# Kernel tuning notes

Hardware: AMD Instinct MI355X
Metric: run time of the kernel (lower is better)

The kernel has to match this reference:

```python
import jax, jax.numpy as jnp
import numpy as np

B, NJ, NM = 64, 30, 20
N = NJ * NM          # 600 operation nodes per FJSP instance
IN_DIM, H = 2, 128


def _bn(h):
    # torch BatchNorm1d in training mode, gamma=1/beta=0 (module init), stats over all nodes
    m = h.mean(axis=(0, 1))
    v = h.var(axis=(0, 1))
    return (h - m) / jnp.sqrt(v + 1e-5)


def setup_inputs() -> dict:
    key = jax.random.key(0)
    ks = jax.random.split(key, 20)
    x = jax.random.normal(ks[0], (B, N, IN_DIM), jnp.float32)
    graph_pool = jnp.full((B, N), 1.0 / N, jnp.float32)   # average graph pooling weights
    padded_nei = jnp.zeros((1,), jnp.int32)               # unused (sum pooling path)
    adj = (jax.random.uniform(ks[1], (B, N, N)) < 0.01).astype(jnp.float32)
    adj = jnp.minimum(adj + jnp.eye(N, dtype=jnp.float32)[None], 1.0)  # self-loops
    candidate = jax.random.randint(ks[2], (B, NJ), 0, N)
    a_index = jax.random.randint(ks[3], (B,), 0, NJ)
    mask = jax.random.uniform(ks[4], (B, NJ)) < 0.2
    mask = mask.at[jnp.arange(B), a_index].set(False)     # chosen action never masked
    mask_mch = jax.random.uniform(ks[5], (B, N, NM)) < 0.3
    dur = jax.random.uniform(ks[6], (B, N, NM), dtype=jnp.float32)
    old_action = jax.random.randint(ks[7], (B,), 0, N)
    mch_pool = jax.random.normal(ks[8], (B, H), jnp.float32)

    def w(k, i, o):
        return jax.random.normal(k, (i, o), jnp.float32) * (1.0 / np.sqrt(i))

    z = lambda n: jnp.zeros((n,), jnp.float32)            # biases init to 0 in module
    return dict(
        x=x, graph_pool=graph_pool, padded_nei=padded_nei, adj=adj,
        candidate=candidate, mask=mask, mask_mch=mask_mch, dur=dur,
        a_index=a_index, old_action=old_action, mch_pool=mch_pool,
        W1_0=w(ks[9], IN_DIM, H), b1_0=z(H), W2_0=w(ks[10], H, H), b2_0=z(H),
        W1_1=w(ks[11], H, H), b1_1=z(H), W2_1=w(ks[12], H, H), b2_1=z(H),
        Wa1=w(ks[13], 3 * H, H), ba1=z(H), Wa2=w(ks[14], H, H), ba2=z(H),
        Wa3=w(ks[15], H, 1), ba3=z(1),
        Wc1=w(ks[16], H, H), bc1=z(H), Wc2=w(ks[17], H, 1), bc2=z(1),
    )


def reference(x, graph_pool, padded_nei, adj, candidate, mask, mask_mch, dur,
              a_index, old_action, mch_pool,
              W1_0, b1_0, W2_0, b2_0, W1_1, b1_1, W2_1, b2_1,
              Wa1, ba1, Wa2, ba2, Wa3, ba3, Wc1, bc1, Wc2, bc2):
    # --- GIN encoder: num_layers-1 = 2 message-passing layers, sum pooling ---
    h = x
    for (W1, b1, W2, b2) in ((W1_0, b1_0, W2_0, b2_0), (W1_1, b1_1, W2_1, b2_1)):
        pooled = jnp.einsum('bnm,bmd->bnd', adj, h)         # neighbor sum (adj has self-loops)
        h1 = jax.nn.relu(_bn(pooled @ W1 + b1))             # MLP hidden (BN inside MLP)
        h = jax.nn.relu(_bn(h1 @ W2 + b2))                  # layer BN + relu
    h_nodes = h                                             # [B, N, H]
    h_pooled = jnp.einsum('bn,bnd->bd', graph_pool, h_nodes)  # [B, H]

    # --- gather candidate features, concat pooled contexts ---
    cand_feat = jnp.take_along_axis(h_nodes, candidate[:, :, None], axis=1)  # [B, NJ, H]
    concat = jnp.concatenate([
        cand_feat,
        jnp.broadcast_to(h_pooled[:, None, :], cand_feat.shape),
        jnp.broadcast_to(mch_pool[:, None, :], cand_feat.shape)], axis=-1)   # [B, NJ, 3H]

    # --- MLPActor(3 layers, tanh) ---
    a = jnp.tanh(concat @ Wa1 + ba1)
    a = jnp.tanh(a @ Wa2 + ba2)
    scores = (a @ Wa3 + ba3).squeeze(-1) * 10.0             # [B, NJ]
    scores = jnp.where(mask, -jnp.inf, scores)
    logpi = jax.nn.log_softmax(scores, axis=1)
    pi = jnp.exp(logpi)
    log_a = jnp.take_along_axis(logpi, a_index[:, None], axis=1)[:, 0]
    entropy = -jnp.sum(jnp.where(pi > 0, pi * logpi, 0.0), axis=1)

    # --- gather action-dependent tensors (detached in torch) ---
    b_idx = jnp.arange(B)
    action_node = dur[b_idx, old_action]                    # [B, NM]
    action_feature = h_nodes[b_idx, old_action]             # [B, H]
    mask_mch_action = mask_mch[b_idx, old_action][:, None, :]  # [B, 1, NM]

    # --- MLPCritic(2 layers, tanh) ---
    v = jnp.tanh(h_pooled @ Wc1 + bc1) @ Wc2 + bc2          # [B, 1]

    sg = jax.lax.stop_gradient
    return (entropy, v, log_a, sg(action_node), sg(action_feature),
            mask_mch_action, sg(h_pooled))
```

## Files before the change

### kernel.cpp

```cpp
#include <hip/hip_runtime.h>
#include <hip/hip_bf16.h>

#define BB 64
#define NJ 30
#define NM 20
#define NN 600
#define HH 128
#define NROWS (BB*NN)
#define CAP 48

typedef __attribute__((ext_vector_type(8))) short short8;
typedef __attribute__((ext_vector_type(4))) float f32x4;

#define STATS_B   0
#define HPOOL_B   4096
#define FLAGS_B   36864
#define ZERO_B    36880
#define WTB_B     37120
#define SCORES_B  135424
#define NBRCNT_B  143104
#define NBRIDX_B  296704
#define CONCAT_B  296704
#define A1_B      3245824
#define POOLED0_B 7669504
#define T1_B      7976704
#define P1_B      27637504

#define OUT_ENT   0
#define OUT_V     64
#define OUT_LOGA  128
#define OUT_ANODE 192
#define OUT_AFEAT 1472
#define OUT_MMCH  9664
#define OUT_HPOOL 10944

__device__ __forceinline__ bool mask_at(const void* p, int layout, long i) {
    if (layout == 2) return ((const float*)p)[i] != 0.f;
    if (layout == 1) return ((const unsigned char*)p)[i] != 0;
    return ((const int*)p)[i] != 0;
}

__device__ __forceinline__ short bf16rne(float f) {
    unsigned u = __float_as_uint(f);
    return (short)((u + 0x7fffu + ((u >> 16) & 1u)) >> 16);
}
__device__ __forceinline__ float bf2f(unsigned h) {
    return __uint_as_float(h << 16);
}
__device__ __forceinline__ unsigned packbf(float a, float b) {
    return ((unsigned)(unsigned short)bf16rne(a)) |
           (((unsigned)(unsigned short)bf16rne(b)) << 16);
}

__global__ __launch_bounds__(256) void k_detect(const void* mask_p, const void* maskmch_p,
                                                int* flags) {
    unsigned agg = 0;
    int which;
    int tid = threadIdx.x;
    if (blockIdx.x == 0) {
        which = 0;
        const unsigned* p = (const unsigned*)mask_p;
        unsigned w0 = (tid < 480) ? p[tid] : 0u;
        unsigned w1 = (tid + 256 < 480) ? p[tid + 256] : 0u;
        agg = w0 | w1;
    } else {
        which = 1;
        const unsigned* p = (const unsigned*)maskmch_p + (size_t)(blockIdx.x - 1) * 800;
        unsigned w0 = p[tid];
        unsigned w1 = (tid + 256 < 800) ? p[tid + 256] : 0u;
        unsigned w2 = (tid + 512 < 800) ? p[tid + 512] : 0u;
        unsigned w3 = (tid + 768 < 800) ? p[tid + 768] : 0u;
        agg = w0 | w1 | w2 | w3;
    }
    int f = 0;
    if (((agg >> 24) & 0xffu) == 0x3fu) f |= 1;
    if ((((agg >> 8) & 0xffu) == 1u) || (((agg >> 16) & 0xffu) == 1u) ||
        (((agg >> 24) & 0xffu) == 1u)) f |= 2;
#pragma unroll
    for (int off = 1; off < 64; off <<= 1) f |= __shfl_xor(f, off);
    if ((tid & 63) == 0 && f) atomicOr(&flags[which], f);
}

__global__ void k_wconv(const float* __restrict__ Wa, const float* __restrict__ Wb,
                        const float* __restrict__ Wc, unsigned short* __restrict__ wT) {
    int mat = blockIdx.x >> 6;
    int idx = ((blockIdx.x & 63) << 8) + threadIdx.x;
    const float* W = mat == 0 ? Wa : (mat == 1 ? Wb : Wc);
    int k = idx >> 7, c = idx & 127;
    wT[mat * 16384 + c * HH + k] = (unsigned short)bf16rne(W[idx]);
}

__global__ __launch_bounds__(256) void k_sparse(const float* __restrict__ adj,
                                                const float* __restrict__ x,
                                                int* __restrict__ nbr_cnt,
                                                int* __restrict__ nbr_idx,
                                                float* __restrict__ pooled0) {
    int wrow = blockIdx.x * 4 + (threadIdx.x >> 6);
    int lane = threadIdx.x & 63;
    int b = wrow / NN;
    const float4* arow = (const float4*)(adj + (size_t)wrow * NN);
    int* irow = nbr_idx + (size_t)wrow * CAP;
    const float* xb = x + (size_t)b * NN * 2;
    float4 vv[3];
    vv[0] = arow[lane];
    vv[1] = arow[64 + lane];
    vv[2] = (128 + lane < 150) ? arow[128 + lane] : make_float4(0.f, 0.f, 0.f, 0.f);
    int cnt = 0;
    float p0 = 0.f, p1 = 0.f;
#pragma unroll
    for (int it = 0; it < 3; ++it) {
        int fi = it * 64 + lane;
#pragma unroll
        for (int s = 0; s < 4; ++s) {
            float c = s == 0 ? vv[it].x : (s == 1 ? vv[it].y : (s == 2 ? vv[it].z : vv[it].w));
            bool pred = (c != 0.f);
            unsigned long long bal = __ballot(pred);
            if (pred) {
                int pos = cnt + __popcll(bal & ((1ull << lane) - 1ull));
                int m = fi * 4 + s;
                if (pos < CAP) irow[pos] = m;
                float2 xv = *(const float2*)&xb[m * 2];
                p0 += xv.x; p1 += xv.y;
            }
            cnt += __popcll(bal);
        }
    }
#pragma unroll
    for (int off = 1; off < 64; off <<= 1) {
        p0 += __shfl_xor(p0, off);
        p1 += __shfl_xor(p1, off);
    }
    if (lane == 0) {
        nbr_cnt[wrow] = cnt < CAP ? cnt : CAP;
        pooled0[(size_t)wrow * 2]     = p0;
        pooled0[(size_t)wrow * 2 + 1] = p1;
    }
}

__global__ __launch_bounds__(256) void k_p0stats(const float* __restrict__ pooled0,
                                                 float* __restrict__ out5) {
    __shared__ float red[4][5];
    int i = blockIdx.x * 256 + threadIdx.x;
    float p0 = pooled0[(size_t)i * 2], p1 = pooled0[(size_t)i * 2 + 1];
    float v[5] = {p0, p1, p0 * p0, p1 * p1, p0 * p1};
#pragma unroll
    for (int j = 0; j < 5; ++j)
#pragma unroll
        for (int off = 1; off < 64; off <<= 1) v[j] += __shfl_xor(v[j], off);
    int lane = threadIdx.x & 63, w = threadIdx.x >> 6;
    if (lane == 0)
#pragma unroll
        for (int j = 0; j < 5; ++j) red[w][j] = v[j];
    __syncthreads();
    if (threadIdx.x == 0)
#pragma unroll
        for (int j = 0; j < 5; ++j)
            atomicAdd(&out5[j], red[0][j] + red[1][j] + red[2][j] + red[3][j]);
}

template<int MODE, int OUTBF>
__global__ __launch_bounds__(256) void k_stage(const void* __restrict__ t_in_v,
                                               const float* __restrict__ pooled0,
                                               const float* __restrict__ W1,
                                               const unsigned short* __restrict__ wT,
                                               const float* __restrict__ stats_in,
                                               void* __restrict__ t_out_v,
                                               float* __restrict__ stats_out) {
    __shared__ float sm_mean[HH], sm_inv[HH];
    __shared__ float smS[4][HH], smQ[4][HH];
    int tid = threadIdx.x;
    if (MODE == 0 && tid < HH) {
        float S0 = stats_in[0], S1 = stats_in[1], Q0 = stats_in[2], Q1 = stats_in[3], P01 = stats_in[4];
        float w0 = W1[tid], w1 = W1[HH + tid];
        float m = (S0 * w0 + S1 * w1) * (1.f / NROWS);
        float eq = (Q0 * w0 * w0 + Q1 * w1 * w1 + 2.f * P01 * w0 * w1) * (1.f / NROWS);
        sm_mean[tid] = m;
        sm_inv[tid] = 1.f / sqrtf(eq - m * m + 1e-5f);
    }
    if (MODE == 1 && tid < HH) {
        float s = stats_in[tid], q = stats_in[HH + tid];
        float m = s * (1.f / NROWS);
        sm_mean[tid] = m;
        sm_inv[tid] = 1.f / sqrtf(q * (1.f / NROWS) - m * m + 1e-5f);
    }
    if (MODE != 2) __syncthreads();

    const unsigned short* tin = (const unsigned short*)t_in_v;
    int lane = tid & 63, wave = tid >> 6;
    int r16 = lane & 15, kg = lane >> 4;
    int rowbase = blockIdx.x * 64 + wave * 16;

    f32x4 acc[8];
#pragma unroll
    for (int t = 0; t < 8; ++t)
#pragma unroll
        for (int i = 0; i < 4; ++i) acc[t][i] = 0.f;

    float p0 = 0.f, p1 = 0.f;
    if (MODE == 0) {
        p0 = pooled0[(size_t)(rowbase + r16) * 2];
        p1 = pooled0[(size_t)(rowbase + r16) * 2 + 1];
    }

#pragma unroll
    for (int ks = 0; ks < 4; ++ks) {
        int kb = ks * 32 + kg * 8;
        short8 afr;
        if (MODE == 2) {
            afr = *(const short8*)&tin[(size_t)(rowbase + r16) * HH + kb];
        } else {
            float av[8];
            if (MODE == 0) {
                float4 wa0 = *(const float4*)&W1[kb];
                float4 wa1 = *(const float4*)&W1[kb + 4];
                float4 wb0 = *(const float4*)&W1[HH + kb];
                float4 wb1 = *(const float4*)&W1[HH + kb + 4];
                av[0] = p0 * wa0.x + p1 * wb0.x; av[1] = p0 * wa0.y + p1 * wb0.y;
                av[2] = p0 * wa0.z + p1 * wb0.z; av[3] = p0 * wa0.w + p1 * wb0.w;
                av[4] = p0 * wa1.x + p1 * wb1.x; av[5] = p0 * wa1.y + p1 * wb1.y;
                av[6] = p0 * wa1.z + p1 * wb1.z; av[7] = p0 * wa1.w + p1 * wb1.w;
            } else {
                short8 raw = *(const short8*)&tin[(size_t)(rowbase + r16) * HH + kb];
#pragma unroll
                for (int j = 0; j < 8; ++j) av[j] = bf2f((unsigned short)raw[j]);
            }
            float4 m0 = *(const float4*)&sm_mean[kb];
            float4 m1 = *(const float4*)&sm_mean[kb + 4];
            float4 i0 = *(const float4*)&sm_inv[kb];
            float4 i1 = *(const float4*)&sm_inv[kb + 4];
            av[0] = fmaxf((av[0] - m0.x) * i0.x, 0.f);
            av[1] = fmaxf((av[1] - m0.y) * i0.y, 0.f);
            av[2] = fmaxf((av[2] - m0.z) * i0.z, 0.f);
            av[3] = fmaxf((av[3] - m0.w) * i0.w, 0.f);
            av[4] = fmaxf((av[4] - m1.x) * i1.x, 0.f);
            av[5] = fmaxf((av[5] - m1.y) * i1.y, 0.f);
            av[6] = fmaxf((av[6] - m1.z) * i1.z, 0.f);
            av[7] = fmaxf((av[7] - m1.w) * i1.w, 0.f);
#pragma unroll
            for (int j = 0; j < 8; ++j) afr[j] = bf16rne(av[j]);
        }
#pragma unroll
        for (int t = 0; t < 8; ++t) {
            short8 bfr = *(const short8*)&wT[(size_t)(t * 16 + r16) * HH + kb];
            acc[t] = __builtin_amdgcn_mfma_f32_16x16x32_bf16(afr, bfr, acc[t], 0, 0, 0);
        }
    }

#pragma unroll
    for (int t = 0; t < 8; ++t) {
        int col = t * 16 + r16;
        float s = 0.f, q = 0.f;
#pragma unroll
        for (int i = 0; i < 4; ++i) {
            float v = acc[t][i];
            if (OUTBF)
                ((unsigned short*)t_out_v)[(size_t)(rowbase + kg * 4 + i) * HH + col] =
                    (unsigned short)bf16rne(v);
            else
                ((float*)t_out_v)[(size_t)(rowbase + kg * 4 + i) * HH + col] = v;
            s += v; q += v * v;
        }
        s += __shfl_xor(s, 16); q += __shfl_xor(q, 16);
        s += __shfl_xor(s, 32); q += __shfl_xor(q, 32);
        if (kg == 0) { smS[wave][col] = s; smQ[wave][col] = q; }
    }
    __syncthreads();
    if (tid < HH) {
        atomicAdd(&stats_out[tid],      smS[0][tid] + smS[1][tid] + smS[2][tid] + smS[3][tid]);
        atomicAdd(&stats_out[HH + tid], smQ[0][tid] + smQ[1][tid] + smQ[2][tid] + smQ[3][tid]);
    }
}

__global__ __launch_bounds__(256) void k_pool1(const unsigned short* __restrict__ t1,
                                               const int* __restrict__ nbr_cnt,
                                               const int* __restrict__ nbr_idx,
                                               const float* __restrict__ stats1,
                                               unsigned short* __restrict__ pooled1) {
    __shared__ float sm_mean[HH], sm_inv[HH];
    int tid = threadIdx.x;
    if (tid < HH) {
        float s = stats1[tid], q = stats1[HH + tid];
        float m = s * (1.f / NROWS);
        sm_mean[tid] = m;
        sm_inv[tid] = 1.f / sqrtf(q * (1.f / NROWS) - m * m + 1e-5f);
    }
    __syncthreads();
    int c4 = tid & 31, rl = tid >> 5;
    int row = blockIdx.x * 8 + rl;
    int b = row / NN;
    float4 mm = *(const float4*)&sm_mean[c4 * 4];
    float4 iv = *(const float4*)&sm_inv[c4 * 4];
    int cnt = nbr_cnt[row];
    const int* ir = nbr_idx + (size_t)row * CAP;
    const unsigned short* tb = t1 + (size_t)b * NN * HH;
    float a0 = 0.f, a1 = 0.f, a2 = 0.f, a3 = 0.f;
    int i = 0;
    for (; i + 1 < cnt; i += 2) {
        int m0 = ir[i], m1 = ir[i + 1];
        uint2 w0 = *(const uint2*)&tb[(size_t)m0 * HH + c4 * 4];
        uint2 w1 = *(const uint2*)&tb[(size_t)m1 * HH + c4 * 4];
        a0 += fmaxf((bf2f(w0.x & 0xffffu) - mm.x) * iv.x, 0.f)
            + fmaxf((bf2f(w1.x & 0xffffu) - mm.x) * iv.x, 0.f);
        a1 += fmaxf((bf2f(w0.x >> 16)     - mm.y) * iv.y, 0.f)
            + fmaxf((bf2f(w1.x >> 16)     - mm.y) * iv.y, 0.f);
        a2 += fmaxf((bf2f(w0.y & 0xffffu) - mm.z) * iv.z, 0.f)
            + fmaxf((bf2f(w1.y & 0xffffu) - mm.z) * iv.z, 0.f);
        a3 += fmaxf((bf2f(w0.y >> 16)     - mm.w) * iv.w, 0.f)
            + fmaxf((bf2f(w1.y >> 16)     - mm.w) * iv.w, 0.f);
    }
    if (i < cnt) {
        int m0 = ir[i];
        uint2 w0 = *(const uint2*)&tb[(size_t)m0 * HH + c4 * 4];
        a0 += fmaxf((bf2f(w0.x & 0xffffu) - mm.x) * iv.x, 0.f);
        a1 += fmaxf((bf2f(w0.x >> 16)     - mm.y) * iv.y, 0.f);
        a2 += fmaxf((bf2f(w0.y & 0xffffu) - mm.z) * iv.z, 0.f);
        a3 += fmaxf((bf2f(w0.y >> 16)     - mm.w) * iv.w, 0.f);
    }
    uint2 o;
    o.x = packbf(a0, a1);
    o.y = packbf(a2, a3);
    *(uint2*)&pooled1[(size_t)row * HH + c4 * 4] = o;
}

__global__ __launch_bounds__(256) void k_hpool(const float* __restrict__ t3,
                                               const float* __restrict__ gp,
                                               const float* __restrict__ stats3,
                                               float* __restrict__ hpool) {
    __shared__ float sm_mean[HH], sm_inv[HH];
    __shared__ float red[256];
    int tid = threadIdx.x;
    if (tid < HH) {
        float s = stats3[tid], q = stats3[HH + tid];
        float m = s * (1.f / NROWS);
        sm_mean[tid] = m;
        sm_inv[tid] = 1.f / sqrtf(q * (1.f / NROWS) - m * m + 1e-5f);
    }
    __syncthreads();
    int b = blockIdx.x >> 3, chunk = blockIdx.x & 7;
    int c = tid & 127, rr = tid >> 7;
    float m = sm_mean[c], iv = sm_inv[c];
    float acc = 0.f;
    for (int n = chunk * 75 + rr; n < chunk * 75 + 75; n += 2) {
        float w = gp[b * NN + n];
        float v = t3[((size_t)b * NN + n) * HH + c];
        acc += w * fmaxf((v - m) * iv, 0.f);
    }
    red[tid] = acc;
    __syncthreads();
    if (tid < HH) atomicAdd(&hpool[b * HH + c], red[c] + red[c + 128]);
}

__global__ __launch_bounds__(128) void k_concat(const float* __restrict__ t3,
                                                const int* __restrict__ cand,
                                                const float* __restrict__ hpool,
                                                const float* __restrict__ mch,
                                                const float* __restrict__ stats3,
                                                float* __restrict__ concat) {
    __shared__ float sm_mean[HH], sm_inv[HH];
    int t = threadIdx.x;
    {
        float s = stats3[t], q = stats3[HH + t];
        float m = s * (1.f / NROWS);
        sm_mean[t] = m;
        sm_inv[t] = 1.f / sqrtf(q * (1.f / NROWS) - m * m + 1e-5f);
    }
    __syncthreads();
    int row = blockIdx.x;
    int b = row / NJ;
    int cd = cand[row];
    float v = t3[((size_t)b * NN + cd) * HH + t];
    concat[(size_t)row * 384 + t]       = fmaxf((v - sm_mean[t]) * sm_inv[t], 0.f);
    concat[(size_t)row * 384 + 128 + t] = hpool[b * HH + t];
    concat[(size_t)row * 384 + 256 + t] = mch[b * HH + t];
}

__global__ __launch_bounds__(256) void k_a1(const float* __restrict__ concat,
                                            const float* __restrict__ Wa1,
                                            const float* __restrict__ ba1,
                                            float* __restrict__ a1out) {
    __shared__ float sh[8 * 384];
    int tid = threadIdx.x;
    int rbase = blockIdx.x * 8;
    const float4* src = (const float4*)(concat + (size_t)rbase * 384);
    float4* dst = (float4*)sh;
    for (int i = tid; i < 768; i += 256) dst[i] = src[i];
    __syncthreads();
    int c = tid & 127, slot = tid >> 7;
    float acc[4] = {0.f, 0.f, 0.f, 0.f};
    for (int k = 0; k < 384; ++k) {
        float w = Wa1[(size_t)k * HH + c];
#pragma unroll
        for (int rr = 0; rr < 4; ++rr)
            acc[rr] += sh[(slot * 4 + rr) * 384 + k] * w;
    }
    float bb = ba1[c];
#pragma unroll
    for (int rr = 0; rr < 4; ++rr)
        a1out[(size_t)(rbase + slot * 4 + rr) * HH + c] = tanhf(acc[rr] + bb);
}

__global__ __launch_bounds__(256) void k_a2s(const float* __restrict__ a1,
                                             const float* __restrict__ Wa2,
                                             const float* __restrict__ ba2,
                                             const float* __restrict__ Wa3,
                                             const float* __restrict__ ba3,
                                             float* __restrict__ scores) {
    __shared__ float sh[8 * HH];
    __shared__ float sred[8][HH];
    int tid = threadIdx.x;
    int rbase = blockIdx.x * 8;
    const float4* src = (const float4*)(a1 + (size_t)rbase * HH);
    float4* dst = (float4*)sh;
    dst[tid] = src[tid];
    __syncthreads();
    int c = tid & 127, slot = tid >> 7;
    float acc[4] = {0.f, 0.f, 0.f, 0.f};
    for (int k = 0; k < HH; ++k) {
        float w = Wa2[(size_t)k * HH + c];
#pragma unroll
        for (int rr = 0; rr < 4; ++rr)
            acc[rr] += sh[(slot * 4 + rr) * HH + k] * w;
    }
    float w3 = Wa3[c], bb = ba2[c];
#pragma unroll
    for (int rr = 0; rr < 4; ++rr)
        sred[slot * 4 + rr][c] = tanhf(acc[rr] + bb) * w3;
    __syncthreads();
    int r = tid >> 5, l32 = tid & 31;
    float v = sred[r][l32] + sred[r][l32 + 32] + sred[r][l32 + 64] + sred[r][l32 + 96];
    v += __shfl_xor(v, 1); v += __shfl_xor(v, 2); v += __shfl_xor(v, 4);
    v += __shfl_xor(v, 8); v += __shfl_xor(v, 16);
    if (l32 == 0) scores[rbase + r] = 10.f * (v + ba3[0]);
}

__global__ __launch_bounds__(128) void k_final(const float* __restrict__ t3,
                                               const float* __restrict__ stats3,
                                               const float* __restrict__ hpool,
                                               const float* __restrict__ scores,
                                               const void* __restrict__ mask_p,
                                               const void* __restrict__ maskmch_p,
                                               const int* __restrict__ flags,
                                               const float* __restrict__ dur,
                                               const int* __restrict__ a_index,
                                               const int* __restrict__ old_action,
                                               const float* __restrict__ Wc1,
                                               const float* __restrict__ bc1,
                                               const float* __restrict__ Wc2,
                                               const float* __restrict__ bc2,
                                               float* __restrict__ out) {
    __shared__ float sm_mean[HH], sm_inv[HH], sh_hp[HH], sh_red[HH];
    __shared__ float sh_s[32], sh_lp[32];
    __shared__ int sh_m[32];
    int b = blockIdx.x, t = threadIdx.x;
    {
        float s = stats3[t], q = stats3[HH + t];
        float m = s * (1.f / NROWS);
        sm_mean[t] = m;
        sm_inv[t] = 1.f / sqrtf(q * (1.f / NROWS) - m * m + 1e-5f);
    }
    sh_hp[t] = hpool[b * HH + t];
    __syncthreads();

    float acc = bc1[t];
    for (int k = 0; k < HH; ++k) acc += sh_hp[k] * Wc1[k * HH + t];
    sh_red[t] = tanhf(acc) * Wc2[t];
    __syncthreads();
    for (int st = 64; st > 0; st >>= 1) {
        if (t < st) sh_red[t] += sh_red[t + st];
        __syncthreads();
    }
    if (t == 0) out[OUT_V + b] = sh_red[0] + bc2[0];

    int fA = flags[0], fB = flags[1];
    int layA = (fA & 1) ? 2 : ((fA & 2) ? 1 : 0);
    int layB = (fB & 1) ? 2 : ((fB & 2) ? 1 : 0);
    if (t < NJ) {
        sh_s[t] = scores[b * NJ + t];
        sh_m[t] = mask_at(mask_p, layA, (long)b * NJ + t) ? 1 : 0;
    }
    __syncthreads();
    if (t == 0) {
        float mx = -1e30f;
        for (int j = 0; j < NJ; ++j)
            if (!sh_m[j] && sh_s[j] > mx) mx = sh_s[j];
        float sum = 0.f;
        for (int j = 0; j < NJ; ++j)
            if (!sh_m[j]) sum += expf(sh_s[j] - mx);
        float lse = mx + logf(sum);
        float ent = 0.f;
        for (int j = 0; j < NJ; ++j) {
            if (!sh_m[j]) {
                float lp = sh_s[j] - lse;
                sh_lp[j] = lp;
                float pi = expf(lp);
                if (pi > 0.f) ent -= pi * lp;
            }
        }
        out[OUT_ENT + b] = ent;
        out[OUT_LOGA + b] = sh_lp[a_index[b]];
    }

    int old = old_action[b];
    if (t < NM) {
        out[OUT_ANODE + b * NM + t] = dur[((size_t)b * NN + old) * NM + t];
        out[OUT_MMCH + b * NM + t] =
            mask_at(maskmch_p, layB, ((size_t)b * NN + old) * NM + t) ? 1.f : 0.f;
    }
    {
        float v = t3[((size_t)b * NN + old) * HH + t];
        out[OUT_AFEAT + b * HH + t] = fmaxf((v - sm_mean[t]) * sm_inv[t], 0.f);
        out[OUT_HPOOL + b * HH + t] = sh_hp[t];
    }
}

extern "C" void kernel_launch(void* const* d_in, const int* in_sizes, int n_in,
                              void* d_out, int out_size, void* d_ws, size_t ws_size,
                              hipStream_t stream) {
    (void)in_sizes; (void)n_in; (void)out_size; (void)ws_size;
    const float* x         = (const float*)d_in[0];
    const float* gp        = (const float*)d_in[1];
    const float* adj       = (const float*)d_in[3];
    const int*   cand      = (const int*)d_in[4];
    const void*  mask_p    = d_in[5];
    const void*  maskmch_p = d_in[6];
    const float* dur       = (const float*)d_in[7];
    const int*   a_index   = (const int*)d_in[8];
    const int*   old_act   = (const int*)d_in[9];
    const float* mch_pool  = (const float*)d_in[10];
    const float* W1_0 = (const float*)d_in[11];
    const float* W2_0 = (const float*)d_in[13];
    const float* W1_1 = (const float*)d_in[15];
    const float* W2_1 = (const float*)d_in[17];
    const float* Wa1  = (const float*)d_in[19];
    const float* ba1  = (const float*)d_in[20];
    const float* Wa2  = (const float*)d_in[21];
    const float* ba2  = (const float*)d_in[22];
    const float* Wa3  = (const float*)d_in[23];
    const float* ba3  = (const float*)d_in[24];
    const float* Wc1  = (const float*)d_in[25];
    const float* bc1  = (const float*)d_in[26];
    const float* Wc2  = (const float*)d_in[27];
    const float* bc2  = (const float*)d_in[28];

    char* ws = (char*)d_ws;
    float* stats   = (float*)(ws + STATS_B);
    float* hpool   = (float*)(ws + HPOOL_B);
    int*   flags   = (int*)(ws + FLAGS_B);
    unsigned short* wtb = (unsigned short*)(ws + WTB_B);
    float* scores  = (float*)(ws + SCORES_B);
    int*   nbr_cnt = (int*)(ws + NBRCNT_B);
    int*   nbr_idx = (int*)(ws + NBRIDX_B);
    float* concat  = (float*)(ws + CONCAT_B);
    float* a1      = (float*)(ws + A1_B);
    float* pooled0 = (float*)(ws + POOLED0_B);
    unsigned short* t1_16 = (unsigned short*)(ws + T1_B);
    unsigned short* p1_16 = (unsigned short*)(ws + P1_B);
    float* t3      = (float*)(ws + P1_B);
    float* out     = (float*)d_out;

    hipMemsetAsync(ws, 0, ZERO_B, stream);
    k_detect<<<25, 256, 0, stream>>>(mask_p, maskmch_p, flags);
    k_wconv<<<192, 256, 0, stream>>>(W2_0, W1_1, W2_1, wtb);
    k_sparse<<<NROWS / 4, 256, 0, stream>>>(adj, x, nbr_cnt, nbr_idx, pooled0);
    k_p0stats<<<NROWS / 256, 256, 0, stream>>>(pooled0, stats);
    k_stage<0, 1><<<600, 256, 0, stream>>>(nullptr, pooled0, W1_0, wtb, stats, t1_16, stats + 256);
    k_pool1<<<NROWS / 8, 256, 0, stream>>>(t1_16, nbr_cnt, nbr_idx, stats + 256, p1_16);
    k_stage<2, 1><<<600, 256, 0, stream>>>(p1_16, nullptr, nullptr, wtb + 16384, stats, t1_16, stats + 512);
    k_stage<1, 0><<<600, 256, 0, stream>>>(t1_16, nullptr, nullptr, wtb + 32768, stats + 512, t3, stats + 768);
    k_hpool<<<BB * 8, 256, 0, stream>>>(t3, gp, stats + 768, hpool);
    k_concat<<<BB * NJ, 128, 0, stream>>>(t3, cand, hpool, mch_pool, stats + 768, concat);
    k_a1<<<240, 256, 0, stream>>>(concat, Wa1, ba1, a1);
    k_a2s<<<240, 256, 0, stream>>>(a1, Wa2, ba2, Wa3, ba3, scores);
    k_final<<<BB, 128, 0, stream>>>(t3, stats + 768, hpool, scores, mask_p, maskmch_p, flags,
                                    dur, a_index, old_act, Wc1, bc1, Wc2, bc2, out);
}
```

Before: 382.3 us.

## Store final stage output as bf16 and fuse actor MLP kernels

```diff
diff --git a/kernel.cpp b/kernel.cpp
--- a/kernel.cpp
+++ b/kernel.cpp
@@ -20,8 +20,6 @@
 #define SCORES_B  135424
 #define NBRCNT_B  143104
 #define NBRIDX_B  296704
-#define CONCAT_B  296704
-#define A1_B      3245824
 #define POOLED0_B 7669504
 #define T1_B      7976704
 #define P1_B      27637504
@@ -158,13 +156,13 @@
             atomicAdd(&out5[j], red[0][j] + red[1][j] + red[2][j] + red[3][j]);
 }
 
-template<int MODE, int OUTBF>
+template<int MODE>
 __global__ __launch_bounds__(256) void k_stage(const void* __restrict__ t_in_v,
                                                const float* __restrict__ pooled0,
                                                const float* __restrict__ W1,
                                                const unsigned short* __restrict__ wT,
                                                const float* __restrict__ stats_in,
-                                               void* __restrict__ t_out_v,
+                                               unsigned short* __restrict__ t_out,
                                                float* __restrict__ stats_out) {
     __shared__ float sm_mean[HH], sm_inv[HH];
     __shared__ float smS[4][HH], smQ[4][HH];
@@ -253,11 +251,7 @@
 #pragma unroll
         for (int i = 0; i < 4; ++i) {
             float v = acc[t][i];
-            if (OUTBF)
-                ((unsigned short*)t_out_v)[(size_t)(rowbase + kg * 4 + i) * HH + col] =
-                    (unsigned short)bf16rne(v);
-            else
-                ((float*)t_out_v)[(size_t)(rowbase + kg * 4 + i) * HH + col] = v;
+            t_out[(size_t)(rowbase + kg * 4 + i) * HH + col] = (unsigned short)bf16rne(v);
             s += v; q += v * v;
         }
         s += __shfl_xor(s, 16); q += __shfl_xor(q, 16);
@@ -322,7 +316,7 @@
     *(uint2*)&pooled1[(size_t)row * HH + c4 * 4] = o;
 }
 
-__global__ __launch_bounds__(256) void k_hpool(const float* __restrict__ t3,
+__global__ __launch_bounds__(256) void k_hpool(const unsigned short* __restrict__ t3,
                                                const float* __restrict__ gp,
                                                const float* __restrict__ stats3,
                                                float* __restrict__ hpool) {
@@ -342,7 +336,7 @@
     float acc = 0.f;
     for (int n = chunk * 75 + rr; n < chunk * 75 + 75; n += 2) {
         float w = gp[b * NN + n];
-        float v = t3[((size_t)b * NN + n) * HH + c];
+        float v = bf2f(t3[((size_t)b * NN + n) * HH + c]);
         acc += w * fmaxf((v - m) * iv, 0.f);
     }
     red[tid] = acc;
@@ -350,81 +344,69 @@
     if (tid < HH) atomicAdd(&hpool[b * HH + c], red[c] + red[c + 128]);
 }
 
-__global__ __launch_bounds__(128) void k_concat(const float* __restrict__ t3,
-                                                const int* __restrict__ cand,
-                                                const float* __restrict__ hpool,
-                                                const float* __restrict__ mch,
-                                                const float* __restrict__ stats3,
-                                                float* __restrict__ concat) {
-    __shared__ float sm_mean[HH], sm_inv[HH];
-    int t = threadIdx.x;
-    {
-        float s = stats3[t], q = stats3[HH + t];
-        float m = s * (1.f / NROWS);
-        sm_mean[t] = m;
-        sm_inv[t] = 1.f / sqrtf(q * (1.f / NROWS) - m * m + 1e-5f);
-    }
-    __syncthreads();
-    int row = blockIdx.x;
-    int b = row / NJ;
-    int cd = cand[row];
-    float v = t3[((size_t)b * NN + cd) * HH + t];
-    concat[(size_t)row * 384 + t]       = fmaxf((v - sm_mean[t]) * sm_inv[t], 0.f);
-    concat[(size_t)row * 384 + 128 + t] = hpool[b * HH + t];
-    concat[(size_t)row * 384 + 256 + t] = mch[b * HH + t];
-}
-
-__global__ __launch_bounds__(256) void k_a1(const float* __restrict__ concat,
-                                            const float* __restrict__ Wa1,
-                                            const float* __restrict__ ba1,
-                                            float* __restrict__ a1out) {
-    __shared__ float sh[8 * 384];
+__global__ __launch_bounds__(256) void k_actor(const unsigned short* __restrict__ t3,
+                                               const int* __restrict__ cand,
+                                               const float* __restrict__ hpool,
+                                               const float* __restrict__ mch,
+                                               const float* __restrict__ stats3,
+                                               const float* __restrict__ Wa1,
+                                               const float* __restrict__ ba1,
+                                               const float* __restrict__ Wa2,
+                                               const float* __restrict__ ba2,
+                                               const float* __restrict__ Wa3,
+                                               const float* __restrict__ ba3,
+                                               float* __restrict__ scores) {
+    __shared__ float sh_c[8 * 384];
+    __shared__ float sh_a1[8 * HH];
+    __shared__ float sred[8][HH];
     int tid = threadIdx.x;
     int rbase = blockIdx.x * 8;
-    const float4* src = (const float4*)(concat + (size_t)rbase * 384);
-    float4* dst = (float4*)sh;
-    for (int i = tid; i < 768; i += 256) dst[i] = src[i];
-    __syncthreads();
     int c = tid & 127, slot = tid >> 7;
+
+    float mean_c, inv_c;
+    {
+        float s = stats3[c], q = stats3[HH + c];
+        float m = s * (1.f / NROWS);
+        mean_c = m;
+        inv_c = 1.f / sqrtf(q * (1.f / NROWS) - m * m + 1e-5f);
+    }
+#pragma unroll
+    for (int rr = 0; rr < 4; ++rr) {
+        int r = slot * 4 + rr;
+        int row = rbase + r;
+        int b = row / NJ;
+        int cd = cand[row];
+        float v = bf2f(t3[((size_t)b * NN + cd) * HH + c]);
+        sh_c[r * 384 + c]       = fmaxf((v - mean_c) * inv_c, 0.f);
+        sh_c[r * 384 + 128 + c] = hpool[b * HH + c];
+        sh_c[r * 384 + 256 + c] = mch[b * HH + c];
+    }
+    __syncthreads();
+
     float acc[4] = {0.f, 0.f, 0.f, 0.f};
     for (int k = 0; k < 384; ++k) {
         float w = Wa1[(size_t)k * HH + c];
 #pragma unroll
         for (int rr = 0; rr < 4; ++rr)
-            acc[rr] += sh[(slot * 4 + rr) * 384 + k] * w;
+            acc[rr] += sh_c[(slot * 4 + rr) * 384 + k] * w;
     }
     float bb = ba1[c];
 #pragma unroll
     for (int rr = 0; rr < 4; ++rr)
-        a1out[(size_t)(rbase + slot * 4 + rr) * HH + c] = tanhf(acc[rr] + bb);
-}
-
-__global__ __launch_bounds__(256) void k_a2s(const float* __restrict__ a1,
-                                             const float* __restrict__ Wa2,
-                                             const float* __restrict__ ba2,
-                                             const float* __restrict__ Wa3,
-                                             const float* __restrict__ ba3,
-                                             float* __restrict__ scores) {
-    __shared__ float sh[8 * HH];
-    __shared__ float sred[8][HH];
-    int tid = threadIdx.x;
-    int rbase = blockIdx.x * 8;
-    const float4* src = (const float4*)(a1 + (size_t)rbase * HH);
-    float4* dst = (float4*)sh;
-    dst[tid] = src[tid];
-    __syncthreads();
-    int c = tid & 127, slot = tid >> 7;
-    float acc[4] = {0.f, 0.f, 0.f, 0.f};
+        sh_a1[(slot * 4 + rr) * HH + c] = tanhf(acc[rr] + bb);
+    __syncthreads();
+
+    float acc2[4] = {0.f, 0.f, 0.f, 0.f};
     for (int k = 0; k < HH; ++k) {
         float w = Wa2[(size_t)k * HH + c];
 #pragma unroll
         for (int rr = 0; rr < 4; ++rr)
-            acc[rr] += sh[(slot * 4 + rr) * HH + k] * w;
-    }
-    float w3 = Wa3[c], bb = ba2[c];
+            acc2[rr] += sh_a1[(slot * 4 + rr) * HH + k] * w;
+    }
+    float w3 = Wa3[c], bb2 = ba2[c];
 #pragma unroll
     for (int rr = 0; rr < 4; ++rr)
-        sred[slot * 4 + rr][c] = tanhf(acc[rr] + bb) * w3;
+        sred[slot * 4 + rr][c] = tanhf(acc2[rr] + bb2) * w3;
     __syncthreads();
     int r = tid >> 5, l32 = tid & 31;
     float v = sred[r][l32] + sred[r][l32 + 32] + sred[r][l32 + 64] + sred[r][l32 + 96];
@@ -433,7 +415,7 @@
     if (l32 == 0) scores[rbase + r] = 10.f * (v + ba3[0]);
 }
 
-__global__ __launch_bounds__(128) void k_final(const float* __restrict__ t3,
+__global__ __launch_bounds__(128) void k_final(const unsigned short* __restrict__ t3,
                                                const float* __restrict__ stats3,
                                                const float* __restrict__ hpool,
                                                const float* __restrict__ scores,
@@ -507,7 +489,7 @@
             mask_at(maskmch_p, layB, ((size_t)b * NN + old) * NM + t) ? 1.f : 0.f;
     }
     {
-        float v = t3[((size_t)b * NN + old) * HH + t];
+        float v = bf2f(t3[((size_t)b * NN + old) * HH + t]);
         out[OUT_AFEAT + b * HH + t] = fmaxf((v - sm_mean[t]) * sm_inv[t], 0.f);
         out[OUT_HPOOL + b * HH + t] = sh_hp[t];
     }
@@ -550,12 +532,9 @@
     float* scores  = (float*)(ws + SCORES_B);
     int*   nbr_cnt = (int*)(ws + NBRCNT_B);
     int*   nbr_idx = (int*)(ws + NBRIDX_B);
-    float* concat  = (float*)(ws + CONCAT_B);
-    float* a1      = (float*)(ws + A1_B);
     float* pooled0 = (float*)(ws + POOLED0_B);
     unsigned short* t1_16 = (unsigned short*)(ws + T1_B);
     unsigned short* p1_16 = (unsigned short*)(ws + P1_B);
-    float* t3      = (float*)(ws + P1_B);
     float* out     = (float*)d_out;
 
     hipMemsetAsync(ws, 0, ZERO_B, stream);
@@ -563,14 +542,14 @@
     k_wconv<<<192, 256, 0, stream>>>(W2_0, W1_1, W2_1, wtb);
     k_sparse<<<NROWS / 4, 256, 0, stream>>>(adj, x, nbr_cnt, nbr_idx, pooled0);
     k_p0stats<<<NROWS / 256, 256, 0, stream>>>(pooled0, stats);
-    k_stage<0, 1><<<600, 256, 0, stream>>>(nullptr, pooled0, W1_0, wtb, stats, t1_16, stats + 256);
+    k_stage<0><<<600, 256, 0, stream>>>(nullptr, pooled0, W1_0, wtb, stats, t1_16, stats + 256);
     k_pool1<<<NROWS / 8, 256, 0, stream>>>(t1_16, nbr_cnt, nbr_idx, stats + 256, p1_16);
-    k_stage<2, 1><<<600, 256, 0, stream>>>(p1_16, nullptr, nullptr, wtb + 16384, stats, t1_16, stats + 512);
-    k_stage<1, 0><<<600, 256, 0, stream>>>(t1_16, nullptr, nullptr, wtb + 32768, stats + 512, t3, stats + 768);
-    k_hpool<<<BB * 8, 256, 0, stream>>>(t3, gp, stats + 768, hpool);
-    k_concat<<<BB * NJ, 128, 0, stream>>>(t3, cand, hpool, mch_pool, stats + 768, concat);
-    k_a1<<<240, 256, 0, stream>>>(concat, Wa1, ba1, a1);
-    k_a2s<<<240, 256, 0, stream>>>(a1, Wa2, ba2, Wa3, ba3, scores);
-    k_final<<<BB, 128, 0, stream>>>(t3, stats + 768, hpool, scores, mask_p, maskmch_p, flags,
+    k_stage<2><<<600, 256, 0, stream>>>(p1_16, nullptr, nullptr, wtb + 16384, stats, t1_16, stats + 512);
+    k_stage<1><<<600, 256, 0, stream>>>(t1_16, nullptr, nullptr, wtb + 32768, stats + 512, p1_16, stats + 768);
+    k_hpool<<<BB * 8, 256, 0, stream>>>(p1_16, gp, stats + 768, hpool);
+    k_actor<<<240, 256, 0, stream>>>(p1_16, cand, hpool, mch_pool, stats + 768,
+                                     Wa1, ba1, Wa2, ba2, Wa3, ba3, scores);
+    k_a_unused_guard: ;
+    k_final<<<BB, 128, 0, stream>>>(p1_16, stats + 768, hpool, scores, mask_p, maskmch_p, flags,
                                     dur, a_index, old_act, Wc1, bc1, Wc2, bc2, out);
 }
```

Measured after the change: 379.9 us. No clear change (-0.6%).
